# Kernel tuning notes

Hardware: AMD Instinct MI355X
Metric: run time of the kernel (lower is better)

Reference implementation:

```python
import jax, jax.numpy as jnp
import numpy as np

BLOCK = 32   # sparsity block size
HO = 128     # out_features // BLOCK
WO = 128     # in_features  // BLOCK
N_TOK = 8192 # batch * seq tokens


def setup_inputs() -> dict:
    key = jax.random.key(0)
    k1, k2 = jax.random.split(key)
    gi, gj = np.meshgrid(np.arange(HO), np.arange(WO), indexing='ij')
    layout = ((gi + gj) % 4 == 0)
    ri, ci = np.nonzero(layout)              # block row/col indices (the LUT)
    nnz = len(ri)                            # 4096 nonzero blocks
    x = jax.random.normal(k1, (N_TOK, WO * BLOCK), dtype=jnp.float32)
    w_blocks = jax.random.normal(k2, (nnz, BLOCK, BLOCK), dtype=jnp.float32) * 0.02
    return {
        "x": x,
        "w_blocks": w_blocks,
        "ri": jnp.asarray(ri, jnp.int32),
        "ci": jnp.asarray(ci, jnp.int32),
    }


def reference(x, w_blocks, ri, ci):
    # DSD block-sparse matmul: y = x @ W^T where W is block-sparse.
    # Scatter the value blocks into the dense [out, in] weight (math-identical
    # to the LUT-driven Triton kernel), then one GEMM.
    Wb = jnp.zeros((HO, WO, BLOCK, BLOCK), dtype=w_blocks.dtype)
    Wb = Wb.at[ri, ci].set(w_blocks)
    W = Wb.transpose(0, 2, 1, 3).reshape(HO * BLOCK, WO * BLOCK)  # [out, in]
    return x @ W.T  # [N_TOK, out]
```

## Files before the change

### kernel.cpp

```cpp
#include <hip/hip_runtime.h>
#include <hip/hip_bf16.h>

#define BLOCK 32
#define HO 128
#define WO 128
#define NTOK 8192
#define NFEAT 4096

typedef __attribute__((ext_vector_type(8))) short short8;
typedef __attribute__((ext_vector_type(4))) float f32x4;

__device__ inline unsigned short f2bf(float f) {
    union { float f; unsigned u; } v; v.f = f;
    unsigned r = v.u + 0x7FFFu + ((v.u >> 16) & 1u);
    return (unsigned short)(r >> 16);
}

__global__ __launch_bounds__(256) void cvt_x(const float* __restrict__ x,
                                             unsigned short* __restrict__ xg) {
    const size_t f8 = ((size_t)blockIdx.x * 256 + threadIdx.x) * 8;
    const int m  = (int)(f8 >> 12);
    const int f  = (int)(f8 & 4095);
    const int cb = f >> 5;
    const int p  = (4 - (cb & 3)) & 3;
    const int dcol = ((cb >> 2) << 5) + (f & 31);
    const float4 v0 = *(const float4*)(x + f8);
    const float4 v1 = *(const float4*)(x + f8 + 4);
    short8 u;
    u[0] = (short)f2bf(v0.x); u[1] = (short)f2bf(v0.y);
    u[2] = (short)f2bf(v0.z); u[3] = (short)f2bf(v0.w);
    u[4] = (short)f2bf(v1.x); u[5] = (short)f2bf(v1.y);
    u[6] = (short)f2bf(v1.z); u[7] = (short)f2bf(v1.w);
    *(short8*)(xg + (size_t)p * NTOK * 1024 + (size_t)m * 1024 + dcol) = u;
}

__global__ __launch_bounds__(256) void cvt_w(const float* __restrict__ w,
                                             unsigned short* __restrict__ wg) {
    const size_t f8 = ((size_t)blockIdx.x * 256 + threadIdx.x) * 8;
    const int bi = (int)(f8 >> 10);
    const int rr = (int)((f8 >> 5) & 31);
    const int cc = (int)(f8 & 31);
    const int ro = bi >> 5, tt = bi & 31;
    const int p  = ro & 3,  A  = ro >> 2;
    const float4 v0 = *(const float4*)(w + f8);
    const float4 v1 = *(const float4*)(w + f8 + 4);
    short8 u;
    u[0] = (short)f2bf(v0.x); u[1] = (short)f2bf(v0.y);
    u[2] = (short)f2bf(v0.z); u[3] = (short)f2bf(v0.w);
    u[4] = (short)f2bf(v1.x); u[5] = (short)f2bf(v1.y);
    u[6] = (short)f2bf(v1.z); u[7] = (short)f2bf(v1.w);
    *(short8*)(wg + (size_t)p * 1024 * 1024 + (size_t)(A * 32 + rr) * 1024
               + tt * 32 + cc) = u;
}

__device__ inline void gld16(const unsigned short* g, unsigned short* l) {
    __builtin_amdgcn_global_load_lds(
        (const __attribute__((address_space(1))) unsigned int*)g,
        (__attribute__((address_space(3))) unsigned int*)l, 16, 0, 0);
}

__global__ __launch_bounds__(256) void gemm_kernel(
    const unsigned short* __restrict__ xg, const unsigned short* __restrict__ wg,
    float* __restrict__ y)
{
    __shared__ unsigned short As[128 * 64];
    __shared__ unsigned short Bs[128 * 64];

    const int p     = blockIdx.z;
    const int mbase = blockIdx.x * 128;
    const int nbase = blockIdx.y * 128;
    const unsigned short* Ab = xg + (size_t)p * NTOK * 1024 + (size_t)mbase * 1024;
    const unsigned short* Bb = wg + (size_t)p * 1024 * 1024 + (size_t)nbase * 1024;

    const int t    = threadIdx.x;
    const int lane = t & 63;
    const int wv   = t >> 6;
    const int wm   = wv >> 1, wn = wv & 1;
    const int lr   = lane & 15;
    const int lk   = (lane >> 4) * 8;
    const int srow = t >> 3;
    const int scol = (t & 7) * 8;

    f32x4 acc[4][4];
    #pragma unroll
    for (int i = 0; i < 4; i++)
        #pragma unroll
        for (int j = 0; j < 4; j++)
            acc[i][j] = (f32x4){0.f, 0.f, 0.f, 0.f};

    for (int ks = 0; ks < 16; ++ks) {
        const int k0 = ks * 64;
        #pragma unroll
        for (int c = 0; c < 4; ++c) {
            const int row = c * 32 + srow;
            gld16(Ab + (size_t)row * 1024 + k0 + scol, &As[row * 64 + scol]);
            gld16(Bb + (size_t)row * 1024 + k0 + scol, &Bs[row * 64 + scol]);
        }
        __syncthreads();

        #pragma unroll
        for (int kk = 0; kk < 2; ++kk) {
            short8 af[4], bf[4];
            #pragma unroll
            for (int i = 0; i < 4; i++)
                af[i] = *(const short8*)&As[(wm * 64 + i * 16 + lr) * 64 + kk * 32 + lk];
            #pragma unroll
            for (int j = 0; j < 4; j++)
                bf[j] = *(const short8*)&Bs[(wn * 64 + j * 16 + lr) * 64 + kk * 32 + lk];
            #pragma unroll
            for (int i = 0; i < 4; i++)
                #pragma unroll
                for (int j = 0; j < 4; j++)
                    acc[i][j] = __builtin_amdgcn_mfma_f32_16x16x32_bf16(af[i], bf[j], acc[i][j], 0, 0, 0);
        }
        __syncthreads();
    }

    #pragma unroll
    for (int i = 0; i < 4; i++) {
        #pragma unroll
        for (int q = 0; q < 4; q++) {
            const int row = mbase + wm * 64 + i * 16 + (lane >> 4) * 4 + q;
            float* yrow = y + (size_t)row * NFEAT;
            #pragma unroll
            for (int j = 0; j < 4; j++) {
                const int n = nbase + wn * 64 + j * 16 + lr;
                const int feat = (p + 4 * (n >> 5)) * 32 + (n & 31);
                yrow[feat] = acc[i][j][q];
            }
        }
    }
}

#define LDA 72
__global__ __launch_bounds__(256) void bsmm_kernel(
    const float* __restrict__ x, const float* __restrict__ w,
    const int* __restrict__ ci, float* __restrict__ y)
{
    __shared__ unsigned short As[128 * LDA];
    __shared__ unsigned short Bs[128 * LDA];
    __shared__ int cis[32];
    const int p = blockIdx.z, ntile = blockIdx.y, mbase = blockIdx.x * 128;
    const int t = threadIdx.x;
    if (t < 32) cis[t] = ci[p * 32 + t];
    const int lane = t & 63, wv = t >> 6, wm = wv >> 1, wn = wv & 1;
    const int lr = lane & 15, lk = (lane >> 4) * 8;
    const int tr = t >> 4, tc4 = (t & 15) * 4, hh = tc4 >> 5, cc = tc4 & 31;
    f32x4 acc[4][4];
    #pragma unroll
    for (int i = 0; i < 4; i++)
        #pragma unroll
        for (int j = 0; j < 4; j++) acc[i][j] = (f32x4){0.f, 0.f, 0.f, 0.f};
    __syncthreads();
    for (int ks = 0; ks < 16; ++ks) {
        const int b0 = ks * 2;
        const int fbase = cis[b0 + hh] * 32 + cc;
        #pragma unroll
        for (int q = 0; q < 8; ++q) {
            const int row = q * 16 + tr;
            const float4 va = *(const float4*)(x + (size_t)(mbase + row) * NFEAT + fbase);
            ushort4 ua; ua.x = f2bf(va.x); ua.y = f2bf(va.y); ua.z = f2bf(va.z); ua.w = f2bf(va.w);
            *(ushort4*)&As[row * LDA + tc4] = ua;
            const int ablk = row >> 5, rr = row & 31;
            const int ro = p + 4 * (ntile * 4 + ablk);
            const int blkidx = ro * 32 + b0 + hh;
            const float4 vb = *(const float4*)(w + (size_t)blkidx * 1024 + rr * 32 + cc);
            ushort4 ub; ub.x = f2bf(vb.x); ub.y = f2bf(vb.y); ub.z = f2bf(vb.z); ub.w = f2bf(vb.w);
            *(ushort4*)&Bs[row * LDA + tc4] = ub;
        }
        __syncthreads();
        #pragma unroll
        for (int kk = 0; kk < 2; ++kk) {
            short8 af[4], bf[4];
            #pragma unroll
            for (int i = 0; i < 4; i++) af[i] = *(const short8*)&As[(wm * 64 + i * 16 + lr) * LDA + kk * 32 + lk];
            #pragma unroll
            for (int j = 0; j < 4; j++) bf[j] = *(const short8*)&Bs[(wn * 64 + j * 16 + lr) * LDA + kk * 32 + lk];
            #pragma unroll
            for (int i = 0; i < 4; i++)
                #pragma unroll
                for (int j = 0; j < 4; j++)
                    acc[i][j] = __builtin_amdgcn_mfma_f32_16x16x32_bf16(af[i], bf[j], acc[i][j], 0, 0, 0);
        }
        __syncthreads();
    }
    #pragma unroll
    for (int i = 0; i < 4; i++)
        #pragma unroll
        for (int q = 0; q < 4; q++) {
            const int row = mbase + wm * 64 + i * 16 + (lane >> 4) * 4 + q;
            float* yrow = y + (size_t)row * NFEAT;
            #pragma unroll
            for (int j = 0; j < 4; j++) {
                const int n = ntile * 128 + wn * 64 + j * 16 + lr;
                const int A = n >> 5, rr2 = n & 31;
                yrow[(p + 4 * A) * 32 + rr2] = acc[i][j][q];
            }
        }
}

extern "C" void kernel_launch(void* const* d_in, const int* in_sizes, int n_in,
                              void* d_out, int out_size, void* d_ws, size_t ws_size,
                              hipStream_t stream) {
    const float* x  = (const float*)d_in[0];
    const float* w  = (const float*)d_in[1];
    const int*   ci = (const int*)d_in[3];
    float* y = (float*)d_out;

    const size_t xg_elems = (size_t)4 * NTOK * 1024;
    const size_t wg_elems = (size_t)4 * 1024 * 1024;
    const size_t need = (xg_elems + wg_elems) * 2;

    if (ws_size >= need) {
        unsigned short* xg = (unsigned short*)d_ws;
        unsigned short* wg = xg + xg_elems;
        hipLaunchKernelGGL(cvt_x, dim3((NTOK * (size_t)NFEAT) / (256 * 8)), dim3(256),
                           0, stream, x, xg);
        hipLaunchKernelGGL(cvt_w, dim3((4096 * 1024) / (256 * 8)), dim3(256),
                           0, stream, w, wg);
        dim3 grid(NTOK / 128, 1024 / 128, 4);
        hipLaunchKernelGGL(gemm_kernel, grid, dim3(256), 0, stream, xg, wg, y);
    } else {
        dim3 grid(NTOK / 128, 8, 4);
        hipLaunchKernelGGL(bsmm_kernel, grid, dim3(256), 0, stream, x, w, ci, y);
    }
}
```

Baseline: 342.9 us.

## Replace GEMM with 256x256 double-buffered 8-wave ping-pong kernel and swizzled layout

Replaces the 128x128 single-buffered GEMM with a 256x256 tile, 512-thread kernel. It double-buffers LDS, splits each K-step into four MFMA quadrants and interleaves global-to-LDS staging with them, using explicit vmcnt/lgkmcnt waits, barriers and setprio. The conversion kernels now write the bf16 operands in a row-XOR-swizzled column order so that the LDS fragment reads avoid bank conflicts. The aim is to hide load latency behind MFMA work and raise data reuse per tile. In exchange it needs more registers and 128KB of LDS per block, and correctness depends on the hand-placed wait counts.

```diff
diff --git a/kernel.cpp b/kernel.cpp
--- a/kernel.cpp
+++ b/kernel.cpp
@@ -16,113 +16,208 @@
     return (unsigned short)(r >> 16);
 }
 
+__device__ __forceinline__ void gld16(const unsigned short* g, unsigned short* l) {
+    __builtin_amdgcn_global_load_lds(
+        (const __attribute__((address_space(1))) unsigned int*)g,
+        (__attribute__((address_space(3))) unsigned int*)l, 16, 0, 0);
+}
+
+#define VMCNT(N) asm volatile("s_waitcnt vmcnt(" #N ")" ::: "memory")
+#define LGKM0 do { asm volatile("s_waitcnt lgkmcnt(0)" ::: "memory"); \
+                   __builtin_amdgcn_sched_barrier(0); } while (0)
+#define BAR() __builtin_amdgcn_s_barrier()
+
 __global__ __launch_bounds__(256) void cvt_x(const float* __restrict__ x,
                                              unsigned short* __restrict__ xg) {
-    const size_t f8 = ((size_t)blockIdx.x * 256 + threadIdx.x) * 8;
-    const int m  = (int)(f8 >> 12);
-    const int f  = (int)(f8 & 4095);
-    const int cb = f >> 5;
-    const int p  = (4 - (cb & 3)) & 3;
-    const int dcol = ((cb >> 2) << 5) + (f & 31);
-    const float4 v0 = *(const float4*)(x + f8);
-    const float4 v1 = *(const float4*)(x + f8 + 4);
+    const size_t d8 = ((size_t)blockIdx.x * 256 + threadIdx.x) * 8;
+    const int p   = (int)(d8 >> 23);
+    const int rem = (int)(d8 & ((1u << 23) - 1));
+    const int m   = rem >> 10;
+    const int dcs = rem & 1023;
+    const int c6  = (dcs & 63) ^ ((m & 4) << 2);
+    const int dcol = (dcs & ~63) | c6;
+    const int kb = dcol >> 5;
+    const int cb = (kb << 2) + ((4 - p) & 3);
+    const int f  = (cb << 5) + (dcol & 31);
+    const float* src = x + (size_t)m * NFEAT + f;
+    const float4 v0 = *(const float4*)src;
+    const float4 v1 = *(const float4*)(src + 4);
     short8 u;
     u[0] = (short)f2bf(v0.x); u[1] = (short)f2bf(v0.y);
     u[2] = (short)f2bf(v0.z); u[3] = (short)f2bf(v0.w);
     u[4] = (short)f2bf(v1.x); u[5] = (short)f2bf(v1.y);
     u[6] = (short)f2bf(v1.z); u[7] = (short)f2bf(v1.w);
-    *(short8*)(xg + (size_t)p * NTOK * 1024 + (size_t)m * 1024 + dcol) = u;
+    *(short8*)(xg + d8) = u;
 }
 
 __global__ __launch_bounds__(256) void cvt_w(const float* __restrict__ w,
                                              unsigned short* __restrict__ wg) {
-    const size_t f8 = ((size_t)blockIdx.x * 256 + threadIdx.x) * 8;
-    const int bi = (int)(f8 >> 10);
-    const int rr = (int)((f8 >> 5) & 31);
-    const int cc = (int)(f8 & 31);
-    const int ro = bi >> 5, tt = bi & 31;
-    const int p  = ro & 3,  A  = ro >> 2;
-    const float4 v0 = *(const float4*)(w + f8);
-    const float4 v1 = *(const float4*)(w + f8 + 4);
+    const size_t d8 = ((size_t)blockIdx.x * 256 + threadIdx.x) * 8;
+    const int p   = (int)(d8 >> 20);
+    const int rem = (int)(d8 & ((1u << 20) - 1));
+    const int n   = rem >> 10;
+    const int kcs = rem & 1023;
+    const int k6  = (kcs & 63) ^ ((n & 4) << 2);
+    const int kcol = (kcs & ~63) | k6;
+    const int tt = kcol >> 5, cc = kcol & 31;
+    const int ro = p + 4 * (n >> 5), rr = n & 31;
+    const int bi = ro * 32 + tt;
+    const float* src = w + (size_t)bi * 1024 + rr * 32 + cc;
+    const float4 v0 = *(const float4*)src;
+    const float4 v1 = *(const float4*)(src + 4);
     short8 u;
     u[0] = (short)f2bf(v0.x); u[1] = (short)f2bf(v0.y);
     u[2] = (short)f2bf(v0.z); u[3] = (short)f2bf(v0.w);
     u[4] = (short)f2bf(v1.x); u[5] = (short)f2bf(v1.y);
     u[6] = (short)f2bf(v1.z); u[7] = (short)f2bf(v1.w);
-    *(short8*)(wg + (size_t)p * 1024 * 1024 + (size_t)(A * 32 + rr) * 1024
-               + tt * 32 + cc) = u;
-}
-
-__device__ inline void gld16(const unsigned short* g, unsigned short* l) {
-    __builtin_amdgcn_global_load_lds(
-        (const __attribute__((address_space(1))) unsigned int*)g,
-        (__attribute__((address_space(3))) unsigned int*)l, 16, 0, 0);
-}
-
-__global__ __launch_bounds__(256) void gemm_kernel(
+    *(short8*)(wg + d8) = u;
+}
+
+template<int QM>
+__device__ __forceinline__ void load_a(short8 (&dst)[4][2], const unsigned short* s,
+                                       int wm, int lr, int kb8, int csw) {
+#pragma unroll
+    for (int i = 0; i < 4; i++)
+#pragma unroll
+        for (int kk = 0; kk < 2; kk++)
+            dst[i][kk] = *(const short8*)&s[(wm * 128 + QM * 64 + i * 16 + lr) * 64
+                                            + ((kk * 32 + kb8) ^ csw)];
+}
+template<int QN>
+__device__ __forceinline__ void load_b(short8 (&dst)[2][2], const unsigned short* s,
+                                       int wn, int lr, int kb8, int csw) {
+#pragma unroll
+    for (int j = 0; j < 2; j++)
+#pragma unroll
+        for (int kk = 0; kk < 2; kk++)
+            dst[j][kk] = *(const short8*)&s[(wn * 64 + QN * 32 + j * 16 + lr) * 64
+                                            + ((kk * 32 + kb8) ^ csw)];
+}
+template<int QM, int QN>
+__device__ __forceinline__ void mfma_quad(f32x4 (&acc)[8][4], const short8 (&a)[4][2],
+                                          const short8 (&b)[2][2]) {
+#pragma unroll
+    for (int i = 0; i < 4; i++)
+#pragma unroll
+        for (int j = 0; j < 2; j++)
+#pragma unroll
+            for (int kk = 0; kk < 2; kk++)
+                acc[QM * 4 + i][QN * 2 + j] = __builtin_amdgcn_mfma_f32_16x16x32_bf16(
+                    a[i][kk], b[j][kk], acc[QM * 4 + i][QN * 2 + j], 0, 0, 0);
+}
+
+__device__ __forceinline__ void stage_half(const unsigned short* gbase,
+                                           unsigned short* lbase,
+                                           int hf, int tt, int sr, int sc) {
+    const int r0 = hf * 128 + sr;
+    gld16(gbase + (size_t)r0 * 1024 + tt * 64 + sc, lbase + r0 * 64 + sc);
+    gld16(gbase + (size_t)(r0 + 8) * 1024 + tt * 64 + sc, lbase + (r0 + 8) * 64 + sc);
+}
+
+__global__ __launch_bounds__(512, 2) void gemm8(
     const unsigned short* __restrict__ xg, const unsigned short* __restrict__ wg,
     float* __restrict__ y)
 {
-    __shared__ unsigned short As[128 * 64];
-    __shared__ unsigned short Bs[128 * 64];
+    __shared__ unsigned short As[2][256 * 64];
+    __shared__ unsigned short Bs[2][256 * 64];
 
     const int p     = blockIdx.z;
-    const int mbase = blockIdx.x * 128;
-    const int nbase = blockIdx.y * 128;
+    const int mbase = blockIdx.x * 256;
+    const int nbase = blockIdx.y * 256;
     const unsigned short* Ab = xg + (size_t)p * NTOK * 1024 + (size_t)mbase * 1024;
     const unsigned short* Bb = wg + (size_t)p * 1024 * 1024 + (size_t)nbase * 1024;
 
     const int t    = threadIdx.x;
     const int lane = t & 63;
     const int wv   = t >> 6;
-    const int wm   = wv >> 1, wn = wv & 1;
+    const int wm   = wv >> 2, wn = wv & 3;
     const int lr   = lane & 15;
-    const int lk   = (lane >> 4) * 8;
-    const int srow = t >> 3;
-    const int scol = (t & 7) * 8;
-
-    f32x4 acc[4][4];
-    #pragma unroll
-    for (int i = 0; i < 4; i++)
-        #pragma unroll
+    const int kb8  = (lane >> 4) * 8;
+    const int csw  = (lr & 4) << 2;
+    const int sr   = wv * 16 + (lane >> 3);
+    const int sc   = (lane & 7) * 8;
+
+    f32x4 acc[8][4];
+#pragma unroll
+    for (int i = 0; i < 8; i++)
+#pragma unroll
         for (int j = 0; j < 4; j++)
             acc[i][j] = (f32x4){0.f, 0.f, 0.f, 0.f};
 
-    for (int ks = 0; ks < 16; ++ks) {
-        const int k0 = ks * 64;
-        #pragma unroll
-        for (int c = 0; c < 4; ++c) {
-            const int row = c * 32 + srow;
-            gld16(Ab + (size_t)row * 1024 + k0 + scol, &As[row * 64 + scol]);
-            gld16(Bb + (size_t)row * 1024 + k0 + scol, &Bs[row * 64 + scol]);
-        }
-        __syncthreads();
-
-        #pragma unroll
-        for (int kk = 0; kk < 2; ++kk) {
-            short8 af[4], bf[4];
-            #pragma unroll
-            for (int i = 0; i < 4; i++)
-                af[i] = *(const short8*)&As[(wm * 64 + i * 16 + lr) * 64 + kk * 32 + lk];
-            #pragma unroll
-            for (int j = 0; j < 4; j++)
-                bf[j] = *(const short8*)&Bs[(wn * 64 + j * 16 + lr) * 64 + kk * 32 + lk];
-            #pragma unroll
-            for (int i = 0; i < 4; i++)
-                #pragma unroll
-                for (int j = 0; j < 4; j++)
-                    acc[i][j] = __builtin_amdgcn_mfma_f32_16x16x32_bf16(af[i], bf[j], acc[i][j], 0, 0, 0);
-        }
-        __syncthreads();
+    short8 a0[4][2], a1[4][2], b0[2][2], b1[2][2];
+
+    stage_half(Ab, &As[0][0], 0, 0, sr, sc);
+    stage_half(Ab, &As[0][0], 1, 0, sr, sc);
+    stage_half(Bb, &Bs[0][0], 0, 0, sr, sc);
+    stage_half(Bb, &Bs[0][0], 1, 0, sr, sc);
+    stage_half(Ab, &As[1][0], 0, 1, sr, sc);
+    VMCNT(2);
+    BAR();
+
+    for (int it = 0; it < 8; ++it) {
+        const int t1 = 2 * it + 1;
+        const int t2 = 2 * it + 2;
+        const int t3 = 2 * it + 3;
+        const bool more = (it < 7);
+
+        load_a<0>(a0, &As[0][0], wm, lr, kb8, csw);
+        load_b<0>(b0, &Bs[0][0], wn, lr, kb8, csw);
+        stage_half(Ab, &As[1][0], 1, t1, sr, sc);
+        BAR(); LGKM0;
+        __builtin_amdgcn_s_setprio(1); mfma_quad<0, 0>(acc, a0, b0); __builtin_amdgcn_s_setprio(0);
+        BAR();
+
+        load_a<1>(a1, &As[0][0], wm, lr, kb8, csw);
+        stage_half(Bb, &Bs[1][0], 0, t1, sr, sc);
+        BAR(); LGKM0;
+        __builtin_amdgcn_s_setprio(1); mfma_quad<1, 0>(acc, a1, b0); __builtin_amdgcn_s_setprio(0);
+        BAR();
+
+        load_b<1>(b1, &Bs[0][0], wn, lr, kb8, csw);
+        stage_half(Bb, &Bs[1][0], 1, t1, sr, sc);
+        BAR(); LGKM0;
+        __builtin_amdgcn_s_setprio(1); mfma_quad<0, 1>(acc, a0, b1); __builtin_amdgcn_s_setprio(0);
+        BAR();
+
+        if (more) stage_half(Ab, &As[0][0], 0, t2, sr, sc);
+        BAR();
+        __builtin_amdgcn_s_setprio(1); mfma_quad<1, 1>(acc, a1, b1); __builtin_amdgcn_s_setprio(0);
+        if (more) VMCNT(2); else VMCNT(0);
+        BAR();
+
+        load_a<0>(a0, &As[1][0], wm, lr, kb8, csw);
+        load_b<0>(b0, &Bs[1][0], wn, lr, kb8, csw);
+        if (more) stage_half(Ab, &As[0][0], 1, t2, sr, sc);
+        BAR(); LGKM0;
+        __builtin_amdgcn_s_setprio(1); mfma_quad<0, 0>(acc, a0, b0); __builtin_amdgcn_s_setprio(0);
+        BAR();
+
+        load_a<1>(a1, &As[1][0], wm, lr, kb8, csw);
+        if (more) stage_half(Bb, &Bs[0][0], 0, t2, sr, sc);
+        BAR(); LGKM0;
+        __builtin_amdgcn_s_setprio(1); mfma_quad<1, 0>(acc, a1, b0); __builtin_amdgcn_s_setprio(0);
+        BAR();
+
+        load_b<1>(b1, &Bs[1][0], wn, lr, kb8, csw);
+        if (more) stage_half(Bb, &Bs[0][0], 1, t2, sr, sc);
+        BAR(); LGKM0;
+        __builtin_amdgcn_s_setprio(1); mfma_quad<0, 1>(acc, a0, b1); __builtin_amdgcn_s_setprio(0);
+        BAR();
+
+        if (more) stage_half(Ab, &As[1][0], 0, t3, sr, sc);
+        BAR();
+        __builtin_amdgcn_s_setprio(1); mfma_quad<1, 1>(acc, a1, b1); __builtin_amdgcn_s_setprio(0);
+        if (more) VMCNT(2);
+        BAR();
     }
 
-    #pragma unroll
-    for (int i = 0; i < 4; i++) {
-        #pragma unroll
+#pragma unroll
+    for (int i = 0; i < 8; i++) {
+#pragma unroll
         for (int q = 0; q < 4; q++) {
-            const int row = mbase + wm * 64 + i * 16 + (lane >> 4) * 4 + q;
+            const int row = mbase + wm * 128 + i * 16 + (lane >> 4) * 4 + q;
             float* yrow = y + (size_t)row * NFEAT;
-            #pragma unroll
+#pragma unroll
             for (int j = 0; j < 4; j++) {
                 const int n = nbase + wn * 64 + j * 16 + lr;
                 const int feat = (p + 4 * (n >> 5)) * 32 + (n & 31);
@@ -147,15 +242,15 @@
     const int lr = lane & 15, lk = (lane >> 4) * 8;
     const int tr = t >> 4, tc4 = (t & 15) * 4, hh = tc4 >> 5, cc = tc4 & 31;
     f32x4 acc[4][4];
-    #pragma unroll
+#pragma unroll
     for (int i = 0; i < 4; i++)
-        #pragma unroll
+#pragma unroll
         for (int j = 0; j < 4; j++) acc[i][j] = (f32x4){0.f, 0.f, 0.f, 0.f};
     __syncthreads();
     for (int ks = 0; ks < 16; ++ks) {
         const int b0 = ks * 2;
         const int fbase = cis[b0 + hh] * 32 + cc;
-        #pragma unroll
+#pragma unroll
         for (int q = 0; q < 8; ++q) {
             const int row = q * 16 + tr;
             const float4 va = *(const float4*)(x + (size_t)(mbase + row) * NFEAT + fbase);
@@ -169,28 +264,28 @@
             *(ushort4*)&Bs[row * LDA + tc4] = ub;
         }
         __syncthreads();
-        #pragma unroll
+#pragma unroll
         for (int kk = 0; kk < 2; ++kk) {
             short8 af[4], bf[4];
-            #pragma unroll
+#pragma unroll
             for (int i = 0; i < 4; i++) af[i] = *(const short8*)&As[(wm * 64 + i * 16 + lr) * LDA + kk * 32 + lk];
-            #pragma unroll
+#pragma unroll
             for (int j = 0; j < 4; j++) bf[j] = *(const short8*)&Bs[(wn * 64 + j * 16 + lr) * LDA + kk * 32 + lk];
-            #pragma unroll
+#pragma unroll
             for (int i = 0; i < 4; i++)
-                #pragma unroll
+#pragma unroll
                 for (int j = 0; j < 4; j++)
                     acc[i][j] = __builtin_amdgcn_mfma_f32_16x16x32_bf16(af[i], bf[j], acc[i][j], 0, 0, 0);
         }
         __syncthreads();
     }
-    #pragma unroll
+#pragma unroll
     for (int i = 0; i < 4; i++)
-        #pragma unroll
+#pragma unroll
         for (int q = 0; q < 4; q++) {
             const int row = mbase + wm * 64 + i * 16 + (lane >> 4) * 4 + q;
             float* yrow = y + (size_t)row * NFEAT;
-            #pragma unroll
+#pragma unroll
             for (int j = 0; j < 4; j++) {
                 const int n = ntile * 128 + wn * 64 + j * 16 + lr;
                 const int A = n >> 5, rr2 = n & 31;
@@ -214,12 +309,12 @@
     if (ws_size >= need) {
         unsigned short* xg = (unsigned short*)d_ws;
         unsigned short* wg = xg + xg_elems;
-        hipLaunchKernelGGL(cvt_x, dim3((NTOK * (size_t)NFEAT) / (256 * 8)), dim3(256),
+        hipLaunchKernelGGL(cvt_x, dim3(((size_t)4 * NTOK * 1024) / (256 * 8)), dim3(256),
                            0, stream, x, xg);
-        hipLaunchKernelGGL(cvt_w, dim3((4096 * 1024) / (256 * 8)), dim3(256),
+        hipLaunchKernelGGL(cvt_w, dim3(((size_t)4 * 1024 * 1024) / (256 * 8)), dim3(256),
                            0, stream, w, wg);
-        dim3 grid(NTOK / 128, 1024 / 128, 4);
-        hipLaunchKernelGGL(gemm_kernel, grid, dim3(256), 0, stream, xg, wg, y);
+        dim3 grid(NTOK / 256, 1024 / 256, 4);
+        hipLaunchKernelGGL(gemm8, grid, dim3(512), 0, stream, xg, wg, y);
     } else {
         dim3 grid(NTOK / 128, 8, 4);
         hipLaunchKernelGGL(bsmm_kernel, grid, dim3(256), 0, stream, x, w, ci, y);
```

Result: faster. 332.3 us (-3.1%).
